# Optimization experiments

Hardware: AMD Instinct MI355X
Metric: run time of the kernel (lower is better)

## Reference

```python
import jax, jax.numpy as jnp
import numpy as np

B, C, H, W, Q = 8, 64, 32, 32, 8
K = 2 ** Q  # codebook size = 256


def setup_inputs() -> dict:
    key = jax.random.key(0)
    k0, k1, k2, k3, k4, k5 = jax.random.split(key, 6)
    x = jax.random.normal(k0, (B, C, H, W), dtype=jnp.float32)
    # grouped 1x1 conv C -> Q*C with groups=C: per-channel weight [C, Q]
    w_pre = jax.random.normal(k1, (C, Q), dtype=jnp.float32) * 0.1
    b_pre = jax.random.normal(k2, (C, Q), dtype=jnp.float32) * 0.01
    # codebook init: uniform(-1/2^Q, 1/2^Q) as in nn.Embedding init in the module
    codebook = jax.random.uniform(k3, (K, Q), dtype=jnp.float32, minval=-1.0 / K, maxval=1.0 / K)
    # grouped 1x1 conv Q*C -> C with groups=C: per-channel weight [C, Q]
    w_after = jax.random.normal(k4, (C, Q), dtype=jnp.float32) * 0.1
    b_after = jax.random.normal(k5, (C,), dtype=jnp.float32) * 0.01
    return {"x": x, "w_pre": w_pre, "b_pre": b_pre, "codebook": codebook,
            "w_after": w_after, "b_after": b_after}


def reference(x, w_pre, b_pre, codebook, w_after, b_after):
    sg = jax.lax.stop_gradient
    Bn, Cn, Hn, Wn = x.shape
    Qn = w_pre.shape[1]
    # pre_quant: grouped 1x1 conv (groups=C): each input channel c -> Q outputs
    # y[b,c,q,h,w] = x[b,c,h,w] * w_pre[c,q] + b_pre[c,q]
    y = x[:, :, None, :, :] * w_pre[None, :, :, None, None] + b_pre[None, :, :, None, None]
    # torch permutes [B, C*Q, H, W] -> [B, H, W, C*Q] then reshapes to (-1, Q);
    # out-channel order is c*Q+q, so rows are (b,h,w,c) blocks of Q features.
    xq = jnp.transpose(y, (0, 3, 4, 1, 2))  # [B, H, W, C, Q]
    flat = xq.reshape(-1, Qn)  # [N, Q]
    cb = codebook  # [K, Q]
    # squared euclidean distances [N, K]
    dist = (jnp.sum(flat * flat, axis=1, keepdims=True)
            + jnp.sum(cb * cb, axis=1)
            - 2.0 * flat @ cb.T)
    idx = jnp.argmin(dist, axis=1)  # [N]
    out = cb[idx]  # gather == one-hot @ codebook, same math
    kl_loss = (jnp.mean((sg(out) - flat) ** 2)
               + 0.25 * jnp.mean((out - sg(flat)) ** 2))
    # straight-through
    bit = flat + sg(out - flat)  # [N, Q]
    bit5 = bit.reshape(Bn, Hn, Wn, Cn, Qn)
    bit_cqhw = jnp.transpose(bit5, (0, 3, 4, 1, 2))  # [B, C, Q, H, W]
    bit_out = bit_cqhw.reshape(Bn, Cn * Qn, Hn, Wn)
    # after_quant: grouped 1x1 conv (groups=C): Q inputs per channel -> 1 output
    recon = (jnp.einsum('bcqhw,cq->bchw', bit_cqhw, w_after)
             + b_after[None, :, None, None])
    return kl_loss, bit_out, recon
```

## Files before the change

kernel.cpp:

```cpp
#include <hip/hip_runtime.h>
#include <float.h>

#define NB 8
#define NC 64
#define NH 32
#define NW 32
#define NQ 8
#define NK 256
#define NROWS (NB*NC*NH*NW)
#define TPB 256
#define RPB 1024
#define NBLK2 (NROWS/RPB)
#define BIT_OFF 1
#define REC_OFF (1 + NROWS*NQ)

#define WS_BREAKS(ws) ((double*)(ws))
#define WS_SEGCB(ws)  ((float*)((char*)(ws) + 196608))
#define WS_SEGR(ws)   ((float*)((char*)(ws) + 720896))
#define WS_SEGBG(ws)  ((double*)((char*)(ws) + 786432))
#define WS_ALPHA(ws)  ((double*)((char*)(ws) + 1048576))
#define WS_M(ws)      ((int*)((char*)(ws) + 1049088))
#define WS_PART(ws)   ((double*)((char*)(ws) + 1049856))

__global__ __launch_bounds__(256) void vq_envelope(
    const float* __restrict__ w_pre,
    const float* __restrict__ b_pre,
    const float* __restrict__ codebook,
    const float* __restrict__ w_after,
    const float* __restrict__ b_after,
    double* __restrict__ g_breaks,
    float* __restrict__ g_segcb,
    float* __restrict__ g_segR,
    double* __restrict__ g_segBG,
    double* __restrict__ g_alpha,
    int* __restrict__ g_m)
{
    __shared__ double2 s_PS[NK];
    __shared__ float   s_cbf[NK][NQ];
    __shared__ double  l_brk[4][NK];
    __shared__ short   l_win[4][NK];
    __shared__ int     s_p[4];

    const int c    = blockIdx.x;
    const int t    = threadIdx.x;
    const int w    = t >> 6;
    const int lane = t & 63;

    double wp[NQ], bp[NQ], wa[NQ];
    double sw2 = 0.0, swb = 0.0, sb2 = 0.0;
    #pragma unroll
    for (int q = 0; q < NQ; q++) {
        wp[q] = (double)w_pre[c*NQ + q];
        bp[q] = (double)b_pre[c*NQ + q];
        wa[q] = (double)w_after[c*NQ + q];
        sw2 = fma(wp[q], wp[q], sw2);
        swb = fma(wp[q], bp[q], swb);
        sb2 = fma(bp[q], bp[q], sb2);
    }
    const double ba = (double)b_after[c];

    {
        double c2 = 0.0, A = 0.0, Bv = 0.0;
        #pragma unroll
        for (int q = 0; q < NQ; q++) {
            const float cf = codebook[t*NQ + q];
            s_cbf[t][q] = cf;
            const double cv = (double)cf;
            c2 = fma(cv, cv, c2);
            A  = fma(wp[q], cv, A);
            Bv = fma(bp[q], cv, Bv);
        }
        s_PS[t] = make_double2(c2 - 2.0*Bv, -2.0*A);
    }
    __syncthreads();

    double P[4], S[4];
    #pragma unroll
    for (int i = 0; i < 4; i++) {
        const double2 ps = s_PS[4*lane + i];
        P[i] = ps.x; S[i] = ps.y;
    }

    const double Ms  = (w == 1) ? -1.0 : (w == 2) ? 0.0125 : 1.0;
    const double Mhi = (w == 0) ? -1.0 : (w == 1) ? 0.0125
                     : (w == 2) ? 1.0  : DBL_MAX;

    int cur;
    if (w == 0) {
        double bs = S[0], bP = P[0];
        int bk = 4*lane;
        #pragma unroll
        for (int i = 1; i < 4; i++) {
            const int k = 4*lane + i;
            if (S[i] > bs || (S[i] == bs && (P[i] < bP || (P[i] == bP && k < bk)))) {
                bs = S[i]; bP = P[i]; bk = k;
            }
        }
        #pragma unroll
        for (int off = 32; off; off >>= 1) {
            double os = __shfl_xor(bs, off, 64);
            double oP = __shfl_xor(bP, off, 64);
            int    ok = __shfl_xor(bk, off, 64);
            if (os > bs || (os == bs && (oP < bP || (oP == bP && ok < bk)))) {
                bs = os; bP = oP; bk = ok;
            }
        }
        cur = bk;
    } else {
        double bd = fma(Ms, S[0], P[0]);
        int bk = 4*lane;
        #pragma unroll
        for (int i = 1; i < 4; i++) {
            const double d = fma(Ms, S[i], P[i]);
            const int k = 4*lane + i;
            if (d < bd || (d == bd && k < bk)) { bd = d; bk = k; }
        }
        #pragma unroll
        for (int off = 32; off; off >>= 1) {
            double od = __shfl_xor(bd, off, 64);
            int    ok = __shfl_xor(bk, off, 64);
            if (od < bd || (od == bd && ok < bk)) { bd = od; bk = ok; }
        }
        cur = bk;
    }

    int p = 0;
    if (w == 0) { if (lane == 0) l_win[0][0] = (short)cur; p = 1; }

    while (p < NK) {
        const double2 psi = s_PS[cur];
        const double Pi = psi.x, Si = psi.y;

        double cx = DBL_MAX, cs = 0.0;
        int cj = NK;
        #pragma unroll
        for (int i = 0; i < 4; i++) {
            const int k = 4*lane + i;
            if (S[i] < Si) {
                const double tt = (P[i] - Pi) / (Si - S[i]);
                if (tt < cx || (tt == cx && (S[i] < cs || (S[i] == cs && k < cj)))) {
                    cx = tt; cs = S[i]; cj = k;
                }
            }
        }
        #pragma unroll
        for (int off = 32; off; off >>= 1) {
            double ox = __shfl_xor(cx, off, 64);
            double os = __shfl_xor(cs, off, 64);
            int    oj = __shfl_xor(cj, off, 64);
            if (ox < cx || (ox == cx && (os < cs || (os == cs && oj < cj)))) {
                cx = ox; cs = os; cj = oj;
            }
        }
        if (cx >= Mhi) break;
        if (lane == 0) {
            l_brk[w][p] = cx;
            l_win[w][p] = (short)cj;
        }
        cur = cj;
        p++;
    }
    if (lane == 0) s_p[w] = p;
    __syncthreads();

    const int o1 = s_p[0];
    const int o2 = o1 + s_p[1];
    const int o3 = o2 + s_p[2];
    const int m  = o3 + s_p[3];

    if (t < m) {
        int w2, s2;
        if      (t < o1) { w2 = 0; s2 = t; }
        else if (t < o2) { w2 = 1; s2 = t - o1; }
        else if (t < o3) { w2 = 2; s2 = t - o2; }
        else             { w2 = 3; s2 = t - o3; }
        const int j = l_win[w2][s2];
        if (t > 0) g_breaks[c*NK + t] = l_brk[w2][s2];
        const double2 ps = s_PS[j];
        double R = ba;
        #pragma unroll
        for (int q = 0; q < NQ; q++) {
            const float cf = s_cbf[j][q];
            g_segcb[(c*NK + t)*NQ + q] = cf;
            R = fma(wa[q], (double)cf, R);
        }
        g_segR[c*NK + t] = (float)R;
        g_segBG[(c*NK + t)*2 + 0] = ps.y + 2.0*swb;
        g_segBG[(c*NK + t)*2 + 1] = ps.x + sb2;
    }
    if (t == 0) {
        g_m[c] = m;
        g_alpha[c] = sw2;
    }
}

__global__ __launch_bounds__(TPB) void vq_main(
    const float* __restrict__ x,
    const double* __restrict__ g_breaks,
    const float* __restrict__ g_segcb,
    const float* __restrict__ g_segR,
    const double* __restrict__ g_segBG,
    const double* __restrict__ g_alpha,
    const int* __restrict__ g_m,
    float* __restrict__ out,
    double* __restrict__ partial)
{
    __shared__ double s_brk[NK];
    __shared__ float  s_cb[NK][9];
    __shared__ float  s_R[NK];
    __shared__ double s_bg[NK][2];
    __shared__ double s_alpha;
    __shared__ double s_part[TPB/64];

    const int tid = threadIdx.x;
    const int bc = blockIdx.x;
    const int b = bc >> 6;
    const int c = bc & 63;
    const int rowbase = bc * RPB;

    const int m = g_m[c];
    if (tid == 0) s_alpha = g_alpha[c];
    if (tid < m) {
        s_brk[tid] = (tid == 0) ? -DBL_MAX : g_breaks[c*NK + tid];
        const float4* cb4 = (const float4*)(g_segcb + (c*NK + tid)*NQ);
        float4 c0 = cb4[0], c1 = cb4[1];
        s_cb[tid][0] = c0.x; s_cb[tid][1] = c0.y; s_cb[tid][2] = c0.z; s_cb[tid][3] = c0.w;
        s_cb[tid][4] = c1.x; s_cb[tid][5] = c1.y; s_cb[tid][6] = c1.z; s_cb[tid][7] = c1.w;
        s_R[tid] = g_segR[c*NK + tid];
        const double2 bg = *(const double2*)(g_segBG + (c*NK + tid)*2);
        s_bg[tid][0] = bg.x; s_bg[tid][1] = bg.y;
    }
    __syncthreads();

    const double alpha = s_alpha;
    const int bq0 = BIT_OFF + (b*512 + c*8)*1024;

    double ktot = 0.0;
    #pragma unroll
    for (int r = 0; r < 4; r++) {
        const int hw  = r*256 + tid;
        const int gid = rowbase + hw;
        const double xv = (double)x[gid];

        int lo = 0, hi = m - 1;
        while (lo < hi) {
            int mid = (lo + hi + 1) >> 1;
            if (s_brk[mid] <= xv) lo = mid; else hi = mid - 1;
        }

        #pragma unroll
        for (int q = 0; q < NQ; q++)
            out[bq0 + q*1024 + hw] = s_cb[lo][q];
        out[REC_OFF + gid] = s_R[lo];

        ktot += fma(xv, fma(xv, alpha, s_bg[lo][0]), s_bg[lo][1]);
    }

    #pragma unroll
    for (int off = 32; off; off >>= 1)
        ktot += __shfl_down(ktot, off, 64);
    if ((tid & 63) == 0) s_part[tid >> 6] = ktot;
    __syncthreads();
    if (tid == 0)
        partial[blockIdx.x] = s_part[0] + s_part[1] + s_part[2] + s_part[3];
}

__global__ __launch_bounds__(TPB) void vq_fin(
    const double* __restrict__ partial,
    float* __restrict__ out)
{
    double s = 0.0;
    for (int i = threadIdx.x; i < NBLK2; i += TPB) s += partial[i];
    #pragma unroll
    for (int off = 32; off; off >>= 1)
        s += __shfl_down(s, off, 64);
    __shared__ double sp[TPB/64];
    if ((threadIdx.x & 63) == 0) sp[threadIdx.x >> 6] = s;
    __syncthreads();
    if (threadIdx.x == 0) {
        double m = (sp[0] + sp[1] + sp[2] + sp[3]) / (double)(NROWS * NQ);
        out[0] = (float)(1.25 * m);
    }
}

extern "C" void kernel_launch(void* const* d_in, const int* in_sizes, int n_in,
                              void* d_out, int out_size, void* d_ws, size_t ws_size,
                              hipStream_t stream) {
    const float* x        = (const float*)d_in[0];
    const float* w_pre    = (const float*)d_in[1];
    const float* b_pre    = (const float*)d_in[2];
    const float* codebook = (const float*)d_in[3];
    const float* w_after  = (const float*)d_in[4];
    const float* b_after  = (const float*)d_in[5];
    float* out = (float*)d_out;

    vq_envelope<<<NC, 256, 0, stream>>>(w_pre, b_pre, codebook, w_after, b_after,
                                        WS_BREAKS(d_ws), WS_SEGCB(d_ws),
                                        WS_SEGR(d_ws), WS_SEGBG(d_ws), WS_ALPHA(d_ws),
                                        WS_M(d_ws));
    vq_main<<<NBLK2, TPB, 0, stream>>>(x, WS_BREAKS(d_ws), WS_SEGCB(d_ws),
                                       WS_SEGR(d_ws), WS_SEGBG(d_ws), WS_ALPHA(d_ws),
                                       WS_M(d_ws), out, WS_PART(d_ws));
    vq_fin<<<1, TPB, 0, stream>>>(WS_PART(d_ws), out);
}
```

Measured before the change: 25.84 us.

## Split envelope walk across 16 waves with data-adaptive slope boundaries

The lower-envelope construction per channel is now split into 16 wavefronts instead of 4. Each wave walks its own slope interval, so the long sequential hull walk becomes shorter per wave. Interval boundaries are placed at quantiles of a fitted Cauchy-like distribution (tan of evenly spaced angles, scaled by statistics of P and S) rather than fixed constants, to balance breakpoints across waves. This adds a block reduction and an extra barrier, uses 1024-thread blocks, and replaces the fixed 4-way segment offset logic with a serial prefix sum.

```diff
diff --git a/kernel.cpp b/kernel.cpp
--- a/kernel.cpp
+++ b/kernel.cpp
@@ -13,6 +13,7 @@
 #define NBLK2 (NROWS/RPB)
 #define BIT_OFF 1
 #define REC_OFF (1 + NROWS*NQ)
+#define NWV 16
 
 #define WS_BREAKS(ws) ((double*)(ws))
 #define WS_SEGCB(ws)  ((float*)((char*)(ws) + 196608))
@@ -22,7 +23,14 @@
 #define WS_M(ws)      ((int*)((char*)(ws) + 1049088))
 #define WS_PART(ws)   ((double*)((char*)(ws) + 1049856))
 
-__global__ __launch_bounds__(256) void vq_envelope(
+__device__ __constant__ double c_tanq[16] = {
+    0.0,
+    -5.027339492125846, -2.414213562373095, -1.496605762665489, -1.0,
+    -0.6681786379192989, -0.41421356237309503, -0.198912367379658, 0.0,
+    0.198912367379658, 0.41421356237309503, 0.6681786379192989, 1.0,
+    1.496605762665489, 2.414213562373095, 5.027339492125846 };
+
+__global__ __launch_bounds__(1024) void vq_envelope(
     const float* __restrict__ w_pre,
     const float* __restrict__ b_pre,
     const float* __restrict__ codebook,
@@ -37,29 +45,32 @@
 {
     __shared__ double2 s_PS[NK];
     __shared__ float   s_cbf[NK][NQ];
-    __shared__ double  l_brk[4][NK];
-    __shared__ short   l_win[4][NK];
-    __shared__ int     s_p[4];
+    __shared__ double  l_brk[NWV][NK];
+    __shared__ short   l_win[NWV][NK];
+    __shared__ int     s_p[NWV];
+    __shared__ int     s_off[NWV + 1];
+    __shared__ double  s_red[4][5];
+    __shared__ double  s_M[NWV];
 
     const int c    = blockIdx.x;
     const int t    = threadIdx.x;
     const int w    = t >> 6;
     const int lane = t & 63;
 
-    double wp[NQ], bp[NQ], wa[NQ];
-    double sw2 = 0.0, swb = 0.0, sb2 = 0.0;
-    #pragma unroll
-    for (int q = 0; q < NQ; q++) {
-        wp[q] = (double)w_pre[c*NQ + q];
-        bp[q] = (double)b_pre[c*NQ + q];
-        wa[q] = (double)w_after[c*NQ + q];
-        sw2 = fma(wp[q], wp[q], sw2);
-        swb = fma(wp[q], bp[q], swb);
-        sb2 = fma(bp[q], bp[q], sb2);
-    }
-    const double ba = (double)b_after[c];
-
-    {
+    double wa[NQ];
+    double sw2 = 0.0, swb = 0.0, sb2 = 0.0, ba = 0.0;
+    if (t < NK) {
+        double wp[NQ], bp[NQ];
+        #pragma unroll
+        for (int q = 0; q < NQ; q++) {
+            wp[q] = (double)w_pre[c*NQ + q];
+            bp[q] = (double)b_pre[c*NQ + q];
+            wa[q] = (double)w_after[c*NQ + q];
+            sw2 = fma(wp[q], wp[q], sw2);
+            swb = fma(wp[q], bp[q], swb);
+            sb2 = fma(bp[q], bp[q], sb2);
+        }
+        ba = (double)b_after[c];
         double c2 = 0.0, A = 0.0, Bv = 0.0;
         #pragma unroll
         for (int q = 0; q < NQ; q++) {
@@ -70,7 +81,41 @@
             A  = fma(wp[q], cv, A);
             Bv = fma(bp[q], cv, Bv);
         }
-        s_PS[t] = make_double2(c2 - 2.0*Bv, -2.0*A);
+        const double Pi = c2 - 2.0*Bv;
+        const double Si = -2.0*A;
+        s_PS[t] = make_double2(Pi, Si);
+
+        double r0 = Pi, r1 = Pi*Pi, r2 = Si, r3 = Si*Si, r4 = Pi*Si;
+        #pragma unroll
+        for (int off = 32; off; off >>= 1) {
+            r0 += __shfl_xor(r0, off, 64);
+            r1 += __shfl_xor(r1, off, 64);
+            r2 += __shfl_xor(r2, off, 64);
+            r3 += __shfl_xor(r3, off, 64);
+            r4 += __shfl_xor(r4, off, 64);
+        }
+        if (lane == 0) {
+            s_red[w][0] = r0; s_red[w][1] = r1; s_red[w][2] = r2;
+            s_red[w][3] = r3; s_red[w][4] = r4;
+        }
+    }
+    __syncthreads();
+
+    if (t == 0) {
+        double sP  = s_red[0][0] + s_red[1][0] + s_red[2][0] + s_red[3][0];
+        double sP2 = s_red[0][1] + s_red[1][1] + s_red[2][1] + s_red[3][1];
+        double sS  = s_red[0][2] + s_red[1][2] + s_red[2][2] + s_red[3][2];
+        double sS2 = s_red[0][3] + s_red[1][3] + s_red[2][3] + s_red[3][3];
+        double sPS = s_red[0][4] + s_red[1][4] + s_red[2][4] + s_red[3][4];
+        const double n = (double)NK;
+        const double mP = sP/n, mS = sS/n;
+        const double vP = fmax(sP2/n - mP*mP, 0.0);
+        const double vS = fmax(sS2/n - mS*mS, 1e-300);
+        const double cv = sPS/n - mP*mS;
+        const double m0 = -cv / vS;
+        const double gm = sqrt(fmax(vP - cv*cv/vS, 0.0) / vS) + 1e-300;
+        #pragma unroll
+        for (int i = 1; i < NWV; i++) s_M[i] = fma(gm, c_tanq[i], m0);
     }
     __syncthreads();
 
@@ -81,9 +126,7 @@
         P[i] = ps.x; S[i] = ps.y;
     }
 
-    const double Ms  = (w == 1) ? -1.0 : (w == 2) ? 0.0125 : 1.0;
-    const double Mhi = (w == 0) ? -1.0 : (w == 1) ? 0.0125
-                     : (w == 2) ? 1.0  : DBL_MAX;
+    const double Mhi = (w == NWV-1) ? DBL_MAX : s_M[w+1];
 
     int cur;
     if (w == 0) {
@@ -107,6 +150,7 @@
         }
         cur = bk;
     } else {
+        const double Ms = s_M[w];
         double bd = fma(Ms, S[0], P[0]);
         int bk = 4*lane;
         #pragma unroll
@@ -163,17 +207,20 @@
     if (lane == 0) s_p[w] = p;
     __syncthreads();
 
-    const int o1 = s_p[0];
-    const int o2 = o1 + s_p[1];
-    const int o3 = o2 + s_p[2];
-    const int m  = o3 + s_p[3];
-
+    if (t == 0) {
+        s_off[0] = 0;
+        #pragma unroll
+        for (int i = 0; i < NWV; i++) s_off[i+1] = s_off[i] + s_p[i];
+        g_m[c] = s_off[NWV];
+        g_alpha[c] = sw2;
+    }
+    __syncthreads();
+
+    const int m = s_off[NWV];
     if (t < m) {
-        int w2, s2;
-        if      (t < o1) { w2 = 0; s2 = t; }
-        else if (t < o2) { w2 = 1; s2 = t - o1; }
-        else if (t < o3) { w2 = 2; s2 = t - o2; }
-        else             { w2 = 3; s2 = t - o3; }
+        int w2 = 0;
+        while (t >= s_off[w2+1]) w2++;
+        const int s2 = t - s_off[w2];
         const int j = l_win[w2][s2];
         if (t > 0) g_breaks[c*NK + t] = l_brk[w2][s2];
         const double2 ps = s_PS[j];
@@ -187,10 +234,6 @@
         g_segR[c*NK + t] = (float)R;
         g_segBG[(c*NK + t)*2 + 0] = ps.y + 2.0*swb;
         g_segBG[(c*NK + t)*2 + 1] = ps.x + sb2;
-    }
-    if (t == 0) {
-        g_m[c] = m;
-        g_alpha[c] = sw2;
     }
 }
 
@@ -294,10 +337,10 @@
     const float* b_after  = (const float*)d_in[5];
     float* out = (float*)d_out;
 
-    vq_envelope<<<NC, 256, 0, stream>>>(w_pre, b_pre, codebook, w_after, b_after,
-                                        WS_BREAKS(d_ws), WS_SEGCB(d_ws),
-                                        WS_SEGR(d_ws), WS_SEGBG(d_ws), WS_ALPHA(d_ws),
-                                        WS_M(d_ws));
+    vq_envelope<<<NC, 1024, 0, stream>>>(w_pre, b_pre, codebook, w_after, b_after,
+                                         WS_BREAKS(d_ws), WS_SEGCB(d_ws),
+                                         WS_SEGR(d_ws), WS_SEGBG(d_ws), WS_ALPHA(d_ws),
+                                         WS_M(d_ws));
     vq_main<<<NBLK2, TPB, 0, stream>>>(x, WS_BREAKS(d_ws), WS_SEGCB(d_ws),
                                        WS_SEGR(d_ws), WS_SEGBG(d_ws), WS_ALPHA(d_ws),
                                        WS_M(d_ws), out, WS_PART(d_ws));
```

Result: faster. 24.43 us (-5.5%).

## Split envelope tracing into 16 quantile windows per channel across separate blocks

Applied to the files above, without the earlier changes.

The lower-envelope construction now runs as 64×16 single-wave blocks. Each block traces the breakpoints inside one slope window, with the window edges placed from statistics of the codebook's (P,S) line parameters using tan-spaced quantiles. This shortens the long serial walk that previously ran in only 4 waves per channel. The main kernel now recomputes the per-codeword outputs itself, picks the window with a linear scan and then binary-searches within it. If any window overflows its fixed slot count, it falls back to a brute-force scan over all 256 codewords, which adds per-block setup work and a slow path in exchange for a shorter critical path in the first kernel.

```diff
diff --git a/kernel.cpp b/kernel.cpp
--- a/kernel.cpp
+++ b/kernel.cpp
@@ -3,48 +3,202 @@
 
 #define NB 8
 #define NC 64
-#define NH 32
-#define NW 32
 #define NQ 8
 #define NK 256
-#define NROWS (NB*NC*NH*NW)
+#define NROWS 524288
 #define TPB 256
 #define RPB 1024
-#define NBLK2 (NROWS/RPB)
+#define NBLK2 512
 #define BIT_OFF 1
 #define REC_OFF (1 + NROWS*NQ)
-
-#define WS_BREAKS(ws) ((double*)(ws))
-#define WS_SEGCB(ws)  ((float*)((char*)(ws) + 196608))
-#define WS_SEGR(ws)   ((float*)((char*)(ws) + 720896))
-#define WS_SEGBG(ws)  ((double*)((char*)(ws) + 786432))
-#define WS_ALPHA(ws)  ((double*)((char*)(ws) + 1048576))
-#define WS_M(ws)      ((int*)((char*)(ws) + 1049088))
-#define WS_PART(ws)   ((double*)((char*)(ws) + 1049856))
-
-__global__ __launch_bounds__(256) void vq_envelope(
+#define NWV 16
+#define SLOT 96
+
+#define WS_BRK(ws)  ((double*)(ws))
+#define WS_WIN(ws)  ((unsigned char*)((char*)(ws) + 786432))
+#define WS_CNT(ws)  ((short*)((char*)(ws) + 884736))
+#define WS_M(ws)    ((double*)((char*)(ws) + 886784))
+#define WS_PART(ws) ((double*)((char*)(ws) + 894976))
+
+__device__ __constant__ double c_tanq[17] = {
+    0.0,
+    -5.027339492125846, -2.414213562373095, -1.496605762665489, -1.0,
+    -0.6681786379192989, -0.41421356237309503, -0.198912367379658, 0.0,
+    0.198912367379658, 0.41421356237309503, 0.6681786379192989, 1.0,
+    1.496605762665489, 2.414213562373095, 5.027339492125846, 0.0 };
+
+__global__ __launch_bounds__(64) void vq_envelope(
+    const float* __restrict__ w_pre,
+    const float* __restrict__ b_pre,
+    const float* __restrict__ codebook,
+    double* __restrict__ g_brk,
+    unsigned char* __restrict__ g_win,
+    short* __restrict__ g_cnt,
+    double* __restrict__ g_M)
+{
+    __shared__ double2 s_PS[NK];
+
+    const int bid  = blockIdx.x;
+    const int c    = bid >> 4;
+    const int w    = bid & 15;
+    const int lane = threadIdx.x;
+
+    double wp[NQ], bp[NQ];
+    #pragma unroll
+    for (int q = 0; q < NQ; q++) {
+        wp[q] = (double)w_pre[c*NQ + q];
+        bp[q] = (double)b_pre[c*NQ + q];
+    }
+
+    double P[4], S[4];
+    double r0 = 0.0, r1 = 0.0, r2 = 0.0, r3 = 0.0, r4 = 0.0;
+    #pragma unroll
+    for (int i = 0; i < 4; i++) {
+        const int k = 4*lane + i;
+        double c2 = 0.0, A = 0.0, Bv = 0.0;
+        #pragma unroll
+        for (int q = 0; q < NQ; q++) {
+            const double cv = (double)codebook[k*NQ + q];
+            c2 = fma(cv, cv, c2);
+            A  = fma(wp[q], cv, A);
+            Bv = fma(bp[q], cv, Bv);
+        }
+        P[i] = c2 - 2.0*Bv;
+        S[i] = -2.0*A;
+        s_PS[k] = make_double2(P[i], S[i]);
+        r0 += P[i]; r1 += P[i]*P[i]; r2 += S[i]; r3 += S[i]*S[i]; r4 += P[i]*S[i];
+    }
+    __syncthreads();
+
+    #pragma unroll
+    for (int off = 32; off; off >>= 1) {
+        r0 += __shfl_xor(r0, off, 64);
+        r1 += __shfl_xor(r1, off, 64);
+        r2 += __shfl_xor(r2, off, 64);
+        r3 += __shfl_xor(r3, off, 64);
+        r4 += __shfl_xor(r4, off, 64);
+    }
+    const double n  = 256.0;
+    const double mP = r0/n, mS = r2/n;
+    const double vP = fmax(r1/n - mP*mP, 0.0);
+    const double vS = fmax(r3/n - mS*mS, 1e-300);
+    const double cv = r4/n - mP*mS;
+    const double m0 = -cv / vS;
+    const double gm = sqrt(fmax(vP - cv*cv/vS, 0.0) / vS) + 1e-300;
+    const double Ms  = fma(gm, c_tanq[w], m0);
+    const double Mhi = (w == NWV-1) ? DBL_MAX : fma(gm, c_tanq[w+1], m0);
+    if (lane == 0) g_M[c*NWV + w] = (w == 0) ? -DBL_MAX : Ms;
+
+    int cur;
+    if (w == 0) {
+        double bs = S[0], bP = P[0];
+        int bk = 4*lane;
+        #pragma unroll
+        for (int i = 1; i < 4; i++) {
+            const int k = 4*lane + i;
+            if (S[i] > bs || (S[i] == bs && (P[i] < bP || (P[i] == bP && k < bk)))) {
+                bs = S[i]; bP = P[i]; bk = k;
+            }
+        }
+        #pragma unroll
+        for (int off = 32; off; off >>= 1) {
+            double os = __shfl_xor(bs, off, 64);
+            double oP = __shfl_xor(bP, off, 64);
+            int    ok = __shfl_xor(bk, off, 64);
+            if (os > bs || (os == bs && (oP < bP || (oP == bP && ok < bk)))) {
+                bs = os; bP = oP; bk = ok;
+            }
+        }
+        cur = bk;
+    } else {
+        double bd = fma(Ms, S[0], P[0]);
+        int bk = 4*lane;
+        #pragma unroll
+        for (int i = 1; i < 4; i++) {
+            const double d = fma(Ms, S[i], P[i]);
+            const int k = 4*lane + i;
+            if (d < bd || (d == bd && k < bk)) { bd = d; bk = k; }
+        }
+        #pragma unroll
+        for (int off = 32; off; off >>= 1) {
+            double od = __shfl_xor(bd, off, 64);
+            int    ok = __shfl_xor(bk, off, 64);
+            if (od < bd || (od == bd && ok < bk)) { bd = od; bk = ok; }
+        }
+        cur = bk;
+    }
+
+    const int gb = (c*NWV + w) * SLOT;
+    if (lane == 0) g_win[gb] = (unsigned char)cur;
+    int p = 1;
+    bool trunc = false;
+
+    while (true) {
+        const double2 psi = s_PS[cur];
+        const double Pi = psi.x, Si = psi.y;
+
+        double cx = DBL_MAX, cs = 0.0;
+        int cj = NK;
+        #pragma unroll
+        for (int i = 0; i < 4; i++) {
+            const int k = 4*lane + i;
+            if (S[i] < Si) {
+                const double tt = (P[i] - Pi) / (Si - S[i]);
+                if (tt < cx || (tt == cx && (S[i] < cs || (S[i] == cs && k < cj)))) {
+                    cx = tt; cs = S[i]; cj = k;
+                }
+            }
+        }
+        #pragma unroll
+        for (int off = 32; off; off >>= 1) {
+            double ox = __shfl_xor(cx, off, 64);
+            double os = __shfl_xor(cs, off, 64);
+            int    oj = __shfl_xor(cj, off, 64);
+            if (ox < cx || (ox == cx && (os < cs || (os == cs && oj < cj)))) {
+                cx = ox; cs = os; cj = oj;
+            }
+        }
+        if (cx >= Mhi) break;
+        if (p >= SLOT) { trunc = true; break; }
+        if (lane == 0) {
+            g_brk[gb + p] = cx;
+            g_win[gb + p] = (unsigned char)cj;
+        }
+        cur = cj;
+        p++;
+    }
+    if (lane == 0) g_cnt[c*NWV + w] = trunc ? (short)-1 : (short)p;
+}
+
+__global__ __launch_bounds__(TPB) void vq_main(
+    const float* __restrict__ x,
     const float* __restrict__ w_pre,
     const float* __restrict__ b_pre,
     const float* __restrict__ codebook,
     const float* __restrict__ w_after,
     const float* __restrict__ b_after,
-    double* __restrict__ g_breaks,
-    float* __restrict__ g_segcb,
-    float* __restrict__ g_segR,
-    double* __restrict__ g_segBG,
-    double* __restrict__ g_alpha,
-    int* __restrict__ g_m)
+    const double* __restrict__ g_brk,
+    const unsigned char* __restrict__ g_win,
+    const short* __restrict__ g_cnt,
+    const double* __restrict__ g_M,
+    float* __restrict__ out,
+    double* __restrict__ partial)
 {
-    __shared__ double2 s_PS[NK];
-    __shared__ float   s_cbf[NK][NQ];
-    __shared__ double  l_brk[4][NK];
-    __shared__ short   l_win[4][NK];
-    __shared__ int     s_p[4];
-
-    const int c    = blockIdx.x;
-    const int t    = threadIdx.x;
-    const int w    = t >> 6;
-    const int lane = t & 63;
+    __shared__ float  s_cb[NK][9];
+    __shared__ float  s_R[NK];
+    __shared__ double s_bg[NK][2];
+    __shared__ double s_brk[NWV*SLOT];
+    __shared__ unsigned char s_win[NWV*SLOT];
+    __shared__ short  s_cnt[NWV];
+    __shared__ double s_M[NWV];
+    __shared__ int    s_bad;
+    __shared__ double s_part[TPB/64];
+
+    const int tid = threadIdx.x;
+    const int bc = blockIdx.x;
+    const int b = bc >> 6;
+    const int c = bc & 63;
+    const int rowbase = bc * RPB;
 
     double wp[NQ], bp[NQ], wa[NQ];
     double sw2 = 0.0, swb = 0.0, sb2 = 0.0;
@@ -58,202 +212,81 @@
         sb2 = fma(bp[q], bp[q], sb2);
     }
     const double ba = (double)b_after[c];
+    const double alpha = sw2;
+
+    if (tid == 0) s_bad = 0;
 
     {
-        double c2 = 0.0, A = 0.0, Bv = 0.0;
+        const float4* cb4 = (const float4*)(codebook + tid*NQ);
+        const float4 c0 = cb4[0], c1 = cb4[1];
+        float cf[NQ] = {c0.x, c0.y, c0.z, c0.w, c1.x, c1.y, c1.z, c1.w};
+        double c2 = 0.0, A = 0.0, Bv = 0.0, R = ba;
         #pragma unroll
         for (int q = 0; q < NQ; q++) {
-            const float cf = codebook[t*NQ + q];
-            s_cbf[t][q] = cf;
-            const double cv = (double)cf;
-            c2 = fma(cv, cv, c2);
-            A  = fma(wp[q], cv, A);
-            Bv = fma(bp[q], cv, Bv);
-        }
-        s_PS[t] = make_double2(c2 - 2.0*Bv, -2.0*A);
+            s_cb[tid][q] = cf[q];
+            const double cvv = (double)cf[q];
+            c2 = fma(cvv, cvv, c2);
+            A  = fma(wp[q], cvv, A);
+            Bv = fma(bp[q], cvv, Bv);
+            R  = fma(wa[q], cvv, R);
+        }
+        const double Pv = c2 - 2.0*Bv;
+        const double Sv = -2.0*A;
+        s_R[tid] = (float)R;
+        s_bg[tid][0] = Sv + 2.0*swb;
+        s_bg[tid][1] = Pv + sb2;
+    }
+    #pragma unroll
+    for (int it = 0; it < (NWV*SLOT)/TPB; it++) {
+        const int idx = it*TPB + tid;
+        const double v = g_brk[c*(NWV*SLOT) + idx];
+        s_brk[idx] = ((idx % SLOT) == 0) ? -DBL_MAX : v;
+        s_win[idx] = g_win[c*(NWV*SLOT) + idx];
+    }
+    if (tid < NWV) {
+        const short cv = g_cnt[c*NWV + tid];
+        s_cnt[tid] = cv;
+        if (cv < 0) s_bad = 1;
+        s_M[tid] = g_M[c*NWV + tid];
     }
     __syncthreads();
-
-    double P[4], S[4];
-    #pragma unroll
-    for (int i = 0; i < 4; i++) {
-        const double2 ps = s_PS[4*lane + i];
-        P[i] = ps.x; S[i] = ps.y;
-    }
-
-    const double Ms  = (w == 1) ? -1.0 : (w == 2) ? 0.0125 : 1.0;
-    const double Mhi = (w == 0) ? -1.0 : (w == 1) ? 0.0125
-                     : (w == 2) ? 1.0  : DBL_MAX;
-
-    int cur;
-    if (w == 0) {
-        double bs = S[0], bP = P[0];
-        int bk = 4*lane;
-        #pragma unroll
-        for (int i = 1; i < 4; i++) {
-            const int k = 4*lane + i;
-            if (S[i] > bs || (S[i] == bs && (P[i] < bP || (P[i] == bP && k < bk)))) {
-                bs = S[i]; bP = P[i]; bk = k;
-            }
-        }
-        #pragma unroll
-        for (int off = 32; off; off >>= 1) {
-            double os = __shfl_xor(bs, off, 64);
-            double oP = __shfl_xor(bP, off, 64);
-            int    ok = __shfl_xor(bk, off, 64);
-            if (os > bs || (os == bs && (oP < bP || (oP == bP && ok < bk)))) {
-                bs = os; bP = oP; bk = ok;
-            }
-        }
-        cur = bk;
-    } else {
-        double bd = fma(Ms, S[0], P[0]);
-        int bk = 4*lane;
-        #pragma unroll
-        for (int i = 1; i < 4; i++) {
-            const double d = fma(Ms, S[i], P[i]);
-            const int k = 4*lane + i;
-            if (d < bd || (d == bd && k < bk)) { bd = d; bk = k; }
-        }
-        #pragma unroll
-        for (int off = 32; off; off >>= 1) {
-            double od = __shfl_xor(bd, off, 64);
-            int    ok = __shfl_xor(bk, off, 64);
-            if (od < bd || (od == bd && ok < bk)) { bd = od; bk = ok; }
-        }
-        cur = bk;
-    }
-
-    int p = 0;
-    if (w == 0) { if (lane == 0) l_win[0][0] = (short)cur; p = 1; }
-
-    while (p < NK) {
-        const double2 psi = s_PS[cur];
-        const double Pi = psi.x, Si = psi.y;
-
-        double cx = DBL_MAX, cs = 0.0;
-        int cj = NK;
-        #pragma unroll
-        for (int i = 0; i < 4; i++) {
-            const int k = 4*lane + i;
-            if (S[i] < Si) {
-                const double tt = (P[i] - Pi) / (Si - S[i]);
-                if (tt < cx || (tt == cx && (S[i] < cs || (S[i] == cs && k < cj)))) {
-                    cx = tt; cs = S[i]; cj = k;
-                }
-            }
-        }
-        #pragma unroll
-        for (int off = 32; off; off >>= 1) {
-            double ox = __shfl_xor(cx, off, 64);
-            double os = __shfl_xor(cs, off, 64);
-            int    oj = __shfl_xor(cj, off, 64);
-            if (ox < cx || (ox == cx && (os < cs || (os == cs && oj < cj)))) {
-                cx = ox; cs = os; cj = oj;
-            }
-        }
-        if (cx >= Mhi) break;
-        if (lane == 0) {
-            l_brk[w][p] = cx;
-            l_win[w][p] = (short)cj;
-        }
-        cur = cj;
-        p++;
-    }
-    if (lane == 0) s_p[w] = p;
-    __syncthreads();
-
-    const int o1 = s_p[0];
-    const int o2 = o1 + s_p[1];
-    const int o3 = o2 + s_p[2];
-    const int m  = o3 + s_p[3];
-
-    if (t < m) {
-        int w2, s2;
-        if      (t < o1) { w2 = 0; s2 = t; }
-        else if (t < o2) { w2 = 1; s2 = t - o1; }
-        else if (t < o3) { w2 = 2; s2 = t - o2; }
-        else             { w2 = 3; s2 = t - o3; }
-        const int j = l_win[w2][s2];
-        if (t > 0) g_breaks[c*NK + t] = l_brk[w2][s2];
-        const double2 ps = s_PS[j];
-        double R = ba;
-        #pragma unroll
-        for (int q = 0; q < NQ; q++) {
-            const float cf = s_cbf[j][q];
-            g_segcb[(c*NK + t)*NQ + q] = cf;
-            R = fma(wa[q], (double)cf, R);
-        }
-        g_segR[c*NK + t] = (float)R;
-        g_segBG[(c*NK + t)*2 + 0] = ps.y + 2.0*swb;
-        g_segBG[(c*NK + t)*2 + 1] = ps.x + sb2;
-    }
-    if (t == 0) {
-        g_m[c] = m;
-        g_alpha[c] = sw2;
-    }
-}
-
-__global__ __launch_bounds__(TPB) void vq_main(
-    const float* __restrict__ x,
-    const double* __restrict__ g_breaks,
-    const float* __restrict__ g_segcb,
-    const float* __restrict__ g_segR,
-    const double* __restrict__ g_segBG,
-    const double* __restrict__ g_alpha,
-    const int* __restrict__ g_m,
-    float* __restrict__ out,
-    double* __restrict__ partial)
-{
-    __shared__ double s_brk[NK];
-    __shared__ float  s_cb[NK][9];
-    __shared__ float  s_R[NK];
-    __shared__ double s_bg[NK][2];
-    __shared__ double s_alpha;
-    __shared__ double s_part[TPB/64];
-
-    const int tid = threadIdx.x;
-    const int bc = blockIdx.x;
-    const int b = bc >> 6;
-    const int c = bc & 63;
-    const int rowbase = bc * RPB;
-
-    const int m = g_m[c];
-    if (tid == 0) s_alpha = g_alpha[c];
-    if (tid < m) {
-        s_brk[tid] = (tid == 0) ? -DBL_MAX : g_breaks[c*NK + tid];
-        const float4* cb4 = (const float4*)(g_segcb + (c*NK + tid)*NQ);
-        float4 c0 = cb4[0], c1 = cb4[1];
-        s_cb[tid][0] = c0.x; s_cb[tid][1] = c0.y; s_cb[tid][2] = c0.z; s_cb[tid][3] = c0.w;
-        s_cb[tid][4] = c1.x; s_cb[tid][5] = c1.y; s_cb[tid][6] = c1.z; s_cb[tid][7] = c1.w;
-        s_R[tid] = g_segR[c*NK + tid];
-        const double2 bg = *(const double2*)(g_segBG + (c*NK + tid)*2);
-        s_bg[tid][0] = bg.x; s_bg[tid][1] = bg.y;
-    }
-    __syncthreads();
-
-    const double alpha = s_alpha;
+    const bool bad = (s_bad != 0);
+
     const int bq0 = BIT_OFF + (b*512 + c*8)*1024;
-
     double ktot = 0.0;
+
     #pragma unroll
     for (int r = 0; r < 4; r++) {
         const int hw  = r*256 + tid;
         const int gid = rowbase + hw;
         const double xv = (double)x[gid];
 
-        int lo = 0, hi = m - 1;
-        while (lo < hi) {
-            int mid = (lo + hi + 1) >> 1;
-            if (s_brk[mid] <= xv) lo = mid; else hi = mid - 1;
+        int j;
+        if (!bad) {
+            int w = 0;
+            #pragma unroll
+            for (int i = 1; i < NWV; i++) w = (s_M[i] <= xv) ? i : w;
+            const int base = w*SLOT;
+            int lo = 0, hi = (int)s_cnt[w] - 1;
+            while (lo < hi) {
+                const int mid = (lo + hi + 1) >> 1;
+                if (s_brk[base + mid] <= xv) lo = mid; else hi = mid - 1;
+            }
+            j = (int)s_win[base + lo];
+        } else {
+            double bd = DBL_MAX; j = 0;
+            for (int k = 0; k < NK; k++) {
+                const double d = fma(xv, s_bg[k][0], s_bg[k][1]);
+                if (d < bd) { bd = d; j = k; }
+            }
         }
 
         #pragma unroll
         for (int q = 0; q < NQ; q++)
-            out[bq0 + q*1024 + hw] = s_cb[lo][q];
-        out[REC_OFF + gid] = s_R[lo];
-
-        ktot += fma(xv, fma(xv, alpha, s_bg[lo][0]), s_bg[lo][1]);
+            out[bq0 + q*1024 + hw] = s_cb[j][q];
+        out[REC_OFF + gid] = s_R[j];
+
+        ktot += fma(xv, fma(xv, alpha, s_bg[j][0]), s_bg[j][1]);
     }
 
     #pragma unroll
@@ -294,12 +327,11 @@
     const float* b_after  = (const float*)d_in[5];
     float* out = (float*)d_out;
 
-    vq_envelope<<<NC, 256, 0, stream>>>(w_pre, b_pre, codebook, w_after, b_after,
-                                        WS_BREAKS(d_ws), WS_SEGCB(d_ws),
-                                        WS_SEGR(d_ws), WS_SEGBG(d_ws), WS_ALPHA(d_ws),
-                                        WS_M(d_ws));
-    vq_main<<<NBLK2, TPB, 0, stream>>>(x, WS_BREAKS(d_ws), WS_SEGCB(d_ws),
-                                       WS_SEGR(d_ws), WS_SEGBG(d_ws), WS_ALPHA(d_ws),
+    vq_envelope<<<NC*NWV, 64, 0, stream>>>(w_pre, b_pre, codebook,
+                                           WS_BRK(d_ws), WS_WIN(d_ws),
+                                           WS_CNT(d_ws), WS_M(d_ws));
+    vq_main<<<NBLK2, TPB, 0, stream>>>(x, w_pre, b_pre, codebook, w_after, b_after,
+                                       WS_BRK(d_ws), WS_WIN(d_ws), WS_CNT(d_ws),
                                        WS_M(d_ws), out, WS_PART(d_ws));
     vq_fin<<<1, TPB, 0, stream>>>(WS_PART(d_ws), out);
 }
```

Result: faster. 22.92 us (-11.3%).
